# Kernel optimization log

Hardware: AMD Instinct MI355X
Metric: run time of the kernel (lower is better)

Reference implementation:

```python
import jax, jax.numpy as jnp
import numpy as np

B, T = 4096, 1024
IN, H, N, OUT = 1, 40, 40, 1  # input_size, hidden_size, nr_nodes, output_size
SLOPE = 0.01  # LeakyReLU negative slope (torch default)


def setup_inputs() -> dict:
    key = jax.random.key(0)
    ks = jax.random.split(key, 9)
    s = lambda fan_in: 1.0 / np.sqrt(fan_in)
    u = lambda k, shape, fan_in: jax.random.uniform(k, shape, jnp.float32, -s(fan_in), s(fan_in))
    return {
        "inputs": jax.random.normal(ks[0], (B, T), dtype=jnp.float32),
        # H2H: Linear(41->40), LeakyReLU, Linear(40->40)
        "h2h_w1": u(ks[1], (N, IN + H), IN + H),
        "h2h_b1": u(ks[2], (N,), IN + H),
        "h2h_w2": u(ks[3], (H, N), N),
        "h2h_b2": u(ks[4], (H,), N),
        # H2O: Linear(41->40), LeakyReLU, Linear(40->1)
        "h2o_w1": u(ks[5], (N, IN + H), IN + H),
        "h2o_b1": u(ks[6], (N,), IN + H),
        "h2o_w2": u(ks[7], (OUT, N), N),
        "h2o_b2": u(ks[8], (OUT,), N),
    }


def reference(inputs, h2h_w1, h2h_b1, h2h_w2, h2h_b2, h2o_w1, h2o_b1, h2o_w2, h2o_b2):
    def step(hidden, u_t):
        # combined: [B, 1+H]
        combined = jnp.concatenate([u_t[:, None], hidden], axis=1)
        a = jax.nn.leaky_relu(combined @ h2h_w1.T + h2h_b1, SLOPE)
        hidden_new = a @ h2h_w2.T + h2h_b2                      # [B, H]
        o = jax.nn.leaky_relu(combined @ h2o_w1.T + h2o_b1, SLOPE)
        out_t = (o @ h2o_w2.T + h2o_b2)[:, 0]                   # [B]
        return hidden_new, out_t

    hidden0 = jnp.zeros((inputs.shape[0], H), dtype=inputs.dtype)
    _, ys = jax.lax.scan(step, hidden0, inputs.T)  # ys: [T, B]
    return ys.T  # [B, T]
```

## Files before the change

### kernel.cpp

```cpp
#include <hip/hip_runtime.h>
#include <hip/hip_bf16.h>


#define B_SZ 4096
#define T_SZ 1024
#define HID  40

typedef unsigned short u16;
typedef unsigned int   u32;
typedef float f2 __attribute__((ext_vector_type(2)));

__device__ __forceinline__ float bf2f(u16 v) {
  union { u32 u; float f; } c; c.u = ((u32)v) << 16; return c.f;
}

template <bool BF>
__device__ __forceinline__ float ldg(const void* p, long i) {
  if (BF) return bf2f(((const u16*)p)[i]);
  return ((const float*)p)[i];
}

template <bool BF>
__device__ __forceinline__ f2 ldg2(const void* p, long i) {
  f2 r;
  r.x = ldg<BF>(p, i + 0);
  r.y = ldg<BF>(p, i + 1);
  return r;
}

__device__ __forceinline__ bool detect_bf16(const void* w) {
  const u16* p = (const u16*)w;
  bool bf = true;
  for (int i = 0; i < 64; ++i) {
    float f = bf2f(p[i]);
    if (!(fabsf(f) <= 0.2f)) bf = false;
  }
  return bf;
}

template <bool BF>
__global__ __launch_bounds__(128, 2)
void rnn_kernel(const void* __restrict__ inp,
                const void* __restrict__ h2h_w1, const void* __restrict__ h2h_b1,
                const void* __restrict__ h2h_w2, const void* __restrict__ h2h_b2,
                const void* __restrict__ h2o_w1, const void* __restrict__ h2o_b1,
                const void* __restrict__ h2o_w2, const void* __restrict__ h2o_b2,
                void* __restrict__ out) {
  __shared__ __align__(16) float sH[4][44];
  __shared__ __align__(16) float sA[4][84];

  if (detect_bf16(h2h_w1) != BF) return;

  const int tid  = threadIdx.x;
  const int lane = tid & 63;
  const int wv   = tid >> 6;
  const int el   = lane & 3;
  const int w    = wv * 16 + (lane >> 2);

  const int a0 = (wv == 0) ? 3 * w : 48 + 2 * (w - 16);
  const int nA = (wv == 0) ? 3 : 2;
  const int rB = (wv == 0) ? ((w < 8) ? 32 + w : ((w == 8) ? 40 : -1)) : 2 * (w - 16);

  f2    wS[4][20];
  float wu[3] = {0, 0, 0}, ba[3] = {0, 0, 0}, bb[2] = {0, 0};
#pragma unroll
  for (int q = 0; q < 3; ++q) {
    if (q < nA) {
      const int  j  = a0 + q;
      const bool hh = (j < HID);
      const void* wb1 = hh ? h2h_w1 : h2o_w1;
      const long  jr  = hh ? j : (j - HID);
      wu[q] = ldg<BF>(wb1, jr * 41);
      ba[q] = ldg<BF>(hh ? h2h_b1 : h2o_b1, jr);
#pragma unroll
      for (int i = 0; i < 20; ++i)
        wS[q][i] = ldg2<BF>(wb1, jr * 41 + 1 + 2 * i);
    }
  }
  if (wv == 0) {
    if (rB >= 0) {
      const bool isout = (rB == 40);
      const void* wb2 = isout ? h2o_w2 : h2h_w2;
      const long  rr  = isout ? 0 : rB;
      bb[0] = isout ? ldg<BF>(h2o_b2, 0) : ldg<BF>(h2h_b2, rB);
#pragma unroll
      for (int i = 0; i < 20; ++i)
        wS[3][i] = ldg2<BF>(wb2, rr * 40 + 2 * i);
    }
  } else {
#pragma unroll
    for (int q = 0; q < 2; ++q) {
      const long r = rB + q;
      bb[q] = ldg<BF>(h2h_b2, r);
#pragma unroll
      for (int i = 0; i < 20; ++i)
        wS[2 + q][i] = ldg2<BF>(h2h_w2, r * 40 + 2 * i);
    }
  }

  for (int i = tid; i < 4 * 44; i += 128) ((float*)sH)[i] = 0.f;
  __syncthreads();

  const int  b    = blockIdx.x * 4 + el;
  const long base = (long)b * T_SZ;
  float u_cur = ldg<BF>(inp, base);

  for (int t = 0; t < T_SZ; ++t) {
    const float u_nxt = (t + 1 < T_SZ) ? ldg<BF>(inp, base + t + 1) : 0.f;

    f2 hv[20];
    {
      const f2* hp = (const f2*)sH[el];
#pragma unroll
      for (int i = 0; i < 20; ++i) hv[i] = hp[i];
    }
#pragma unroll
    for (int q = 0; q < 3; ++q) {
      if (q < nA) {
        f2 acc = {0.f, 0.f};
#pragma unroll
        for (int i = 0; i < 20; ++i)
          acc = hv[i] * wS[q][i] + acc;
        const float a = fmaf(u_cur, wu[q], ba[q]) + acc.x + acc.y;
        sA[el][a0 + q] = fmaxf(a, 0.01f * a);
      }
    }
    __syncthreads();

    if (wv == 1) {
      f2 av[20];
      {
        const f2* ap = (const f2*)sA[el];
#pragma unroll
        for (int i = 0; i < 20; ++i) av[i] = ap[i];
      }
#pragma unroll
      for (int q = 0; q < 2; ++q) {
        f2 acc = {0.f, 0.f};
#pragma unroll
        for (int i = 0; i < 20; ++i)
          acc = av[i] * wS[2 + q][i] + acc;
        sH[el][rB + q] = bb[q] + acc.x + acc.y;
      }
    } else if (rB >= 0) {
      const f2* ap = (const f2*)(&sA[el][(rB == 40) ? 40 : 0]);
      f2 av[20];
#pragma unroll
      for (int i = 0; i < 20; ++i) av[i] = ap[i];
      f2 acc = {0.f, 0.f};
#pragma unroll
      for (int i = 0; i < 20; ++i)
        acc = av[i] * wS[3][i] + acc;
      const float a2 = bb[0] + acc.x + acc.y;
      if (rB < HID) {
        sH[el][rB] = a2;
      } else {
        if (BF) ((__hip_bfloat16*)out)[base + t] = __float2bfloat16(a2);
        else    ((float*)out)[base + t] = a2;
      }
    }
    __syncthreads();

    u_cur = u_nxt;
  }
}

extern "C" void kernel_launch(void* const* d_in, const int* in_sizes, int n_in,
                              void* d_out, int out_size, void* d_ws, size_t ws_size,
                              hipStream_t stream) {
  (void)in_sizes; (void)n_in; (void)out_size; (void)d_ws; (void)ws_size;
  rnn_kernel<false><<<dim3(B_SZ / 4), dim3(128), 0, stream>>>(
      d_in[0], d_in[1], d_in[2], d_in[3], d_in[4],
      d_in[5], d_in[6], d_in[7], d_in[8], d_out);
  rnn_kernel<true><<<dim3(B_SZ / 4), dim3(128), 0, stream>>>(
      d_in[0], d_in[1], d_in[2], d_in[3], d_in[4],
      d_in[5], d_in[6], d_in[7], d_in[8], d_out);
}
```

Measured before the change: 742.7 us.

## Redistribute RNN matvec work across 256 threads per block with fewer rows each

Doubles the block from 128 to 256 threads, still covering 4 batch elements, and reassigns work. Each thread now computes one or two first-layer rows instead of two or three, and one second-layer row instead of up to two. This shortens the serial dependency chain per timestep and cuts register use, using split accumulators and hidden-state values read directly from shared memory. In exchange there are twice as many wavefronts per block synchronising every step, and some threads in the upper waves sit idle during the second phase.

```diff
diff --git a/kernel.cpp b/kernel.cpp
--- a/kernel.cpp
+++ b/kernel.cpp
@@ -39,7 +39,7 @@
 }
 
 template <bool BF>
-__global__ __launch_bounds__(128, 2)
+__global__ __launch_bounds__(256, 4)
 void rnn_kernel(const void* __restrict__ inp,
                 const void* __restrict__ h2h_w1, const void* __restrict__ h2h_b1,
                 const void* __restrict__ h2h_w2, const void* __restrict__ h2h_b2,
@@ -51,112 +51,103 @@
 
   if (detect_bf16(h2h_w1) != BF) return;
 
-  const int tid  = threadIdx.x;
-  const int lane = tid & 63;
-  const int wv   = tid >> 6;
-  const int el   = lane & 3;
-  const int w    = wv * 16 + (lane >> 2);
+  const int tid = threadIdx.x;
+  const int el  = tid & 3;
+  const int w   = tid >> 2;
+  const int wv  = tid >> 6;
+  const bool two = (wv == 0);
 
-  const int a0 = (wv == 0) ? 3 * w : 48 + 2 * (w - 16);
-  const int nA = (wv == 0) ? 3 : 2;
-  const int rB = (wv == 0) ? ((w < 8) ? 32 + w : ((w == 8) ? 40 : -1)) : 2 * (w - 16);
-
-  f2    wS[4][20];
-  float wu[3] = {0, 0, 0}, ba[3] = {0, 0, 0}, bb[2] = {0, 0};
+  f2    wS0[20];
+  float wu0, ba0;
+  {
+    const bool hh = (w < HID);
+    const void* w1p = hh ? h2h_w1 : h2o_w1;
+    const long  jr  = hh ? w : (w - HID);
+    wu0 = ldg<BF>(w1p, jr * 41);
+    ba0 = ldg<BF>(hh ? h2h_b1 : h2o_b1, jr);
 #pragma unroll
-  for (int q = 0; q < 3; ++q) {
-    if (q < nA) {
-      const int  j  = a0 + q;
-      const bool hh = (j < HID);
-      const void* wb1 = hh ? h2h_w1 : h2o_w1;
-      const long  jr  = hh ? j : (j - HID);
-      wu[q] = ldg<BF>(wb1, jr * 41);
-      ba[q] = ldg<BF>(hh ? h2h_b1 : h2o_b1, jr);
-#pragma unroll
-      for (int i = 0; i < 20; ++i)
-        wS[q][i] = ldg2<BF>(wb1, jr * 41 + 1 + 2 * i);
-    }
-  }
-  if (wv == 0) {
-    if (rB >= 0) {
-      const bool isout = (rB == 40);
-      const void* wb2 = isout ? h2o_w2 : h2h_w2;
-      const long  rr  = isout ? 0 : rB;
-      bb[0] = isout ? ldg<BF>(h2o_b2, 0) : ldg<BF>(h2h_b2, rB);
-#pragma unroll
-      for (int i = 0; i < 20; ++i)
-        wS[3][i] = ldg2<BF>(wb2, rr * 40 + 2 * i);
-    }
-  } else {
-#pragma unroll
-    for (int q = 0; q < 2; ++q) {
-      const long r = rB + q;
-      bb[q] = ldg<BF>(h2h_b2, r);
-#pragma unroll
-      for (int i = 0; i < 20; ++i)
-        wS[2 + q][i] = ldg2<BF>(h2h_w2, r * 40 + 2 * i);
-    }
+    for (int i = 0; i < 20; ++i)
+      wS0[i] = ldg2<BF>(w1p, jr * 41 + 1 + 2 * i);
   }
 
-  for (int i = tid; i < 4 * 44; i += 128) ((float*)sH)[i] = 0.f;
+  f2    wS1[20];
+  float wuX = 0.f, baX = 0.f, bbX = 0.f;
+#pragma unroll
+  for (int i = 0; i < 20; ++i) wS1[i] = (f2)0.f;
+  if (two) {
+    const long jr = 24 + w;
+    wuX = ldg<BF>(h2o_w1, jr * 41);
+    baX = ldg<BF>(h2o_b1, jr);
+#pragma unroll
+    for (int i = 0; i < 20; ++i)
+      wS1[i] = ldg2<BF>(h2o_w1, jr * 41 + 1 + 2 * i);
+  } else if (w <= 56) {
+    const bool isout = (w == 56);
+    const void* w2p = isout ? h2o_w2 : h2h_w2;
+    const long  rr  = isout ? 0 : (w - 16);
+    bbX = isout ? ldg<BF>(h2o_b2, 0) : ldg<BF>(h2h_b2, w - 16);
+#pragma unroll
+    for (int i = 0; i < 20; ++i)
+      wS1[i] = ldg2<BF>(w2p, rr * 40 + 2 * i);
+  }
+
+  for (int i = tid; i < 4 * 44; i += 256) ((float*)sH)[i] = 0.f;
   __syncthreads();
 
   const int  b    = blockIdx.x * 4 + el;
   const long base = (long)b * T_SZ;
   float u_cur = ldg<BF>(inp, base);
 
+  const f2* hp = (const f2*)sH[el];
+
   for (int t = 0; t < T_SZ; ++t) {
     const float u_nxt = (t + 1 < T_SZ) ? ldg<BF>(inp, base + t + 1) : 0.f;
 
-    f2 hv[20];
+    f2 ac00 = {0.f, 0.f}, ac01 = {0.f, 0.f};
+    f2 ac10 = {0.f, 0.f}, ac11 = {0.f, 0.f};
+#pragma unroll
+    for (int m = 0; m < 5; ++m) {
+      const f2 h0 = hp[4 * m + 0], h1 = hp[4 * m + 1];
+      const f2 h2 = hp[4 * m + 2], h3 = hp[4 * m + 3];
+      ac00 = h0 * wS0[4 * m + 0] + ac00;
+      ac00 = h1 * wS0[4 * m + 1] + ac00;
+      ac01 = h2 * wS0[4 * m + 2] + ac01;
+      ac01 = h3 * wS0[4 * m + 3] + ac01;
+      if (two) {
+        ac10 = h0 * wS1[4 * m + 0] + ac10;
+        ac10 = h1 * wS1[4 * m + 1] + ac10;
+        ac11 = h2 * wS1[4 * m + 2] + ac11;
+        ac11 = h3 * wS1[4 * m + 3] + ac11;
+      }
+    }
     {
-      const f2* hp = (const f2*)sH[el];
-#pragma unroll
-      for (int i = 0; i < 20; ++i) hv[i] = hp[i];
+      const float a0 = fmaf(u_cur, wu0, ba0) + ac00.x + ac00.y + ac01.x + ac01.y;
+      sA[el][w] = fmaxf(a0, 0.01f * a0);
     }
-#pragma unroll
-    for (int q = 0; q < 3; ++q) {
-      if (q < nA) {
-        f2 acc = {0.f, 0.f};
-#pragma unroll
-        for (int i = 0; i < 20; ++i)
-          acc = hv[i] * wS[q][i] + acc;
-        const float a = fmaf(u_cur, wu[q], ba[q]) + acc.x + acc.y;
-        sA[el][a0 + q] = fmaxf(a, 0.01f * a);
-      }
+    if (two) {
+      const float a1 = fmaf(u_cur, wuX, baX) + ac10.x + ac10.y + ac11.x + ac11.y;
+      sA[el][64 + w] = fmaxf(a1, 0.01f * a1);
     }
     __syncthreads();
 
-    if (wv == 1) {
-      f2 av[20];
-      {
-        const f2* ap = (const f2*)sA[el];
+    if (!two && w <= 56) {
+      const f2* ap = (const f2*)(&sA[el][(w == 56) ? 40 : 0]);
+      f2 bc0 = {0.f, 0.f}, bc1 = {0.f, 0.f};
 #pragma unroll
-        for (int i = 0; i < 20; ++i) av[i] = ap[i];
+      for (int m = 0; m < 5; ++m) {
+        const f2 a0 = ap[4 * m + 0], a1 = ap[4 * m + 1];
+        const f2 a2 = ap[4 * m + 2], a3 = ap[4 * m + 3];
+        bc0 = a0 * wS1[4 * m + 0] + bc0;
+        bc0 = a1 * wS1[4 * m + 1] + bc0;
+        bc1 = a2 * wS1[4 * m + 2] + bc1;
+        bc1 = a3 * wS1[4 * m + 3] + bc1;
       }
-#pragma unroll
-      for (int q = 0; q < 2; ++q) {
-        f2 acc = {0.f, 0.f};
-#pragma unroll
-        for (int i = 0; i < 20; ++i)
-          acc = av[i] * wS[2 + q][i] + acc;
-        sH[el][rB + q] = bb[q] + acc.x + acc.y;
-      }
-    } else if (rB >= 0) {
-      const f2* ap = (const f2*)(&sA[el][(rB == 40) ? 40 : 0]);
-      f2 av[20];
-#pragma unroll
-      for (int i = 0; i < 20; ++i) av[i] = ap[i];
-      f2 acc = {0.f, 0.f};
-#pragma unroll
-      for (int i = 0; i < 20; ++i)
-        acc = av[i] * wS[3][i] + acc;
-      const float a2 = bb[0] + acc.x + acc.y;
-      if (rB < HID) {
-        sH[el][rB] = a2;
+      const float v = bbX + bc0.x + bc0.y + bc1.x + bc1.y;
+      if (w < 56) {
+        sH[el][w - 16] = v;
       } else {
-        if (BF) ((__hip_bfloat16*)out)[base + t] = __float2bfloat16(a2);
-        else    ((float*)out)[base + t] = a2;
+        if (BF) ((__hip_bfloat16*)out)[base + t] = __float2bfloat16(v);
+        else    ((float*)out)[base + t] = v;
       }
     }
     __syncthreads();
@@ -169,10 +160,10 @@
                               void* d_out, int out_size, void* d_ws, size_t ws_size,
                               hipStream_t stream) {
   (void)in_sizes; (void)n_in; (void)out_size; (void)d_ws; (void)ws_size;
-  rnn_kernel<false><<<dim3(B_SZ / 4), dim3(128), 0, stream>>>(
+  rnn_kernel<false><<<dim3(B_SZ / 4), dim3(256), 0, stream>>>(
       d_in[0], d_in[1], d_in[2], d_in[3], d_in[4],
       d_in[5], d_in[6], d_in[7], d_in[8], d_out);
-  rnn_kernel<true><<<dim3(B_SZ / 4), dim3(128), 0, stream>>>(
+  rnn_kernel<true><<<dim3(B_SZ / 4), dim3(256), 0, stream>>>(
       d_in[0], d_in[1], d_in[2], d_in[3], d_in[4],
       d_in[5], d_in[6], d_in[7], d_in[8], d_out);
 }
```

Result: slower. 1.903 ms (+156.3%).

## Map one batch row per block with split-K pairs and DPP reduction

Applied to the files above, without the earlier changes.

Each block now handles a single batch element instead of four. Each pair of threads splits the 40-wide dot products in half and combines the halves with a DPP lane swap. Part of the output branch's first layer (rows 24-39) moves into the second phase, with the final output projection deferred one step and double-buffered hidden and output state, to balance work across the two barriers. This shortens each thread's serial chain per timestep, at the cost of four times as many blocks, more redundant weight loads per block, and lower batch reuse of the register-held weights.

```diff
diff --git a/kernel.cpp b/kernel.cpp
--- a/kernel.cpp
+++ b/kernel.cpp
@@ -38,6 +38,11 @@
   return bf;
 }
 
+__device__ __forceinline__ float pair_other(float x) {
+  return __int_as_float(__builtin_amdgcn_update_dpp(
+      0, __float_as_int(x), 0xB1, 0xF, 0xF, true));
+}
+
 template <bool BF>
 __global__ __launch_bounds__(128, 2)
 void rnn_kernel(const void* __restrict__ inp,
@@ -46,122 +51,129 @@
                 const void* __restrict__ h2o_w1, const void* __restrict__ h2o_b1,
                 const void* __restrict__ h2o_w2, const void* __restrict__ h2o_b2,
                 void* __restrict__ out) {
-  __shared__ __align__(16) float sH[4][44];
-  __shared__ __align__(16) float sA[4][84];
+  __shared__ __align__(16) float sH[2][40];
+  __shared__ __align__(16) float sA[44];
+  __shared__ __align__(16) float sO[2][40];
 
   if (detect_bf16(h2h_w1) != BF) return;
 
   const int tid  = threadIdx.x;
-  const int lane = tid & 63;
-  const int wv   = tid >> 6;
-  const int el   = lane & 3;
-  const int w    = wv * 16 + (lane >> 2);
+  const int kh   = tid & 1;
+  const int p    = tid >> 1;
+  const int koff = kh * 20;
 
-  const int a0 = (wv == 0) ? 3 * w : 48 + 2 * (w - 16);
-  const int nA = (wv == 0) ? 3 : 2;
-  const int rB = (wv == 0) ? ((w < 8) ? 32 + w : ((w == 8) ? 40 : -1)) : 2 * (w - 16);
-
-  f2    wS[4][20];
-  float wu[3] = {0, 0, 0}, ba[3] = {0, 0, 0}, bb[2] = {0, 0};
+  f2    w1s[10];
+  float wu1, ba1;
+  {
+    const bool hh = (p < HID);
+    const void* wp = hh ? h2h_w1 : h2o_w1;
+    const long  jr = hh ? p : (p - HID);
+    wu1 = (kh == 0) ? ldg<BF>(wp, jr * 41) : 0.f;
+    ba1 = (kh == 0) ? ldg<BF>(hh ? h2h_b1 : h2o_b1, jr) : 0.f;
 #pragma unroll
-  for (int q = 0; q < 3; ++q) {
-    if (q < nA) {
-      const int  j  = a0 + q;
-      const bool hh = (j < HID);
-      const void* wb1 = hh ? h2h_w1 : h2o_w1;
-      const long  jr  = hh ? j : (j - HID);
-      wu[q] = ldg<BF>(wb1, jr * 41);
-      ba[q] = ldg<BF>(hh ? h2h_b1 : h2o_b1, jr);
-#pragma unroll
-      for (int i = 0; i < 20; ++i)
-        wS[q][i] = ldg2<BF>(wb1, jr * 41 + 1 + 2 * i);
-    }
-  }
-  if (wv == 0) {
-    if (rB >= 0) {
-      const bool isout = (rB == 40);
-      const void* wb2 = isout ? h2o_w2 : h2h_w2;
-      const long  rr  = isout ? 0 : rB;
-      bb[0] = isout ? ldg<BF>(h2o_b2, 0) : ldg<BF>(h2h_b2, rB);
-#pragma unroll
-      for (int i = 0; i < 20; ++i)
-        wS[3][i] = ldg2<BF>(wb2, rr * 40 + 2 * i);
-    }
-  } else {
-#pragma unroll
-    for (int q = 0; q < 2; ++q) {
-      const long r = rB + q;
-      bb[q] = ldg<BF>(h2h_b2, r);
-#pragma unroll
-      for (int i = 0; i < 20; ++i)
-        wS[2 + q][i] = ldg2<BF>(h2h_w2, r * 40 + 2 * i);
-    }
+    for (int i = 0; i < 10; ++i)
+      w1s[i] = ldg2<BF>(wp, jr * 41 + 1 + koff + 2 * i);
   }
 
-  for (int i = tid; i < 4 * 44; i += 128) ((float*)sH)[i] = 0.f;
+  f2    w2s[10];
+  float wu2 = 0.f, bb2 = 0.f;
+#pragma unroll
+  for (int i = 0; i < 10; ++i) w2s[i] = (f2)0.f;
+  if (p < HID) {
+    if (kh == 0) bb2 = ldg<BF>(h2h_b2, p);
+#pragma unroll
+    for (int i = 0; i < 10; ++i)
+      w2s[i] = ldg2<BF>(h2h_w2, (long)p * HID + koff + 2 * i);
+  } else if (p < 56) {
+    const long jr = 24 + (p - 40);
+    if (kh == 0) { wu2 = ldg<BF>(h2o_w1, jr * 41); bb2 = ldg<BF>(h2o_b1, jr); }
+#pragma unroll
+    for (int i = 0; i < 10; ++i)
+      w2s[i] = ldg2<BF>(h2o_w1, jr * 41 + 1 + koff + 2 * i);
+  } else if (p == 56) {
+    if (kh == 0) bb2 = ldg<BF>(h2o_b2, 0);
+#pragma unroll
+    for (int i = 0; i < 10; ++i)
+      w2s[i] = ldg2<BF>(h2o_w2, koff + 2 * i);
+  }
+
+  for (int i = tid; i < 80; i += 128) { ((float*)sH)[i] = 0.f; ((float*)sO)[i] = 0.f; }
+  if (tid < 44) sA[tid] = 0.f;
   __syncthreads();
 
-  const int  b    = blockIdx.x * 4 + el;
-  const long base = (long)b * T_SZ;
+  const long base = (long)blockIdx.x * T_SZ;
   float u_cur = ldg<BF>(inp, base);
 
+  const f2* h_rd0 = (const f2*)(&sH[0][koff]);
+  const f2* h_rd1 = (const f2*)(&sH[1][koff]);
+  float* w1p0 = (p < HID) ? &sA[p] : &sO[0][p - HID];
+  float* w1p1 = (p < HID) ? &sA[p] : &sO[1][p - HID];
+  const f2* r20 = (p < HID)  ? (const f2*)(&sA[koff])
+                : (p < 56)   ? (const f2*)(&sH[0][koff])
+                : (p == 56)  ? (const f2*)(&sO[1][koff])
+                             : (const f2*)(&sA[koff]);
+  const f2* r21 = (p < HID)  ? (const f2*)(&sA[koff])
+                : (p < 56)   ? (const f2*)(&sH[1][koff])
+                : (p == 56)  ? (const f2*)(&sO[0][koff])
+                             : (const f2*)(&sA[koff]);
+  float* w2p0 = (p < HID) ? &sH[1][p] : (p < 56 ? &sO[0][24 + (p - 40)] : &sA[40]);
+  float* w2p1 = (p < HID) ? &sH[0][p] : (p < 56 ? &sO[1][24 + (p - 40)] : &sA[40]);
+  const bool leaky2 = (p >= HID) && (p < 56);
+  const bool wr2    = (kh == 0) && (p < 56);
+  const bool wrY    = (kh == 0) && (p == 56);
+
   for (int t = 0; t < T_SZ; ++t) {
+    const bool odd = (t & 1);
     const float u_nxt = (t + 1 < T_SZ) ? ldg<BF>(inp, base + t + 1) : 0.f;
 
-    f2 hv[20];
     {
-      const f2* hp = (const f2*)sH[el];
+      const f2* hp = odd ? h_rd1 : h_rd0;
+      f2 hv[10];
 #pragma unroll
-      for (int i = 0; i < 20; ++i) hv[i] = hp[i];
-    }
+      for (int i = 0; i < 10; ++i) hv[i] = hp[i];
+      f2 acc = {0.f, 0.f};
 #pragma unroll
-    for (int q = 0; q < 3; ++q) {
-      if (q < nA) {
-        f2 acc = {0.f, 0.f};
-#pragma unroll
-        for (int i = 0; i < 20; ++i)
-          acc = hv[i] * wS[q][i] + acc;
-        const float a = fmaf(u_cur, wu[q], ba[q]) + acc.x + acc.y;
-        sA[el][a0 + q] = fmaxf(a, 0.01f * a);
-      }
+      for (int i = 0; i < 10; ++i) acc = hv[i] * w1s[i] + acc;
+      const float s1 = fmaf(u_cur, wu1, ba1) + acc.x + acc.y;
+      const float t1 = s1 + pair_other(s1);
+      const float a1 = fmaxf(t1, 0.01f * t1);
+      if (kh == 0) *(odd ? w1p1 : w1p0) = a1;
     }
     __syncthreads();
 
-    if (wv == 1) {
-      f2 av[20];
-      {
-        const f2* ap = (const f2*)sA[el];
+    {
+      const f2* rp = odd ? r21 : r20;
+      f2 av[10];
 #pragma unroll
-        for (int i = 0; i < 20; ++i) av[i] = ap[i];
-      }
-#pragma unroll
-      for (int q = 0; q < 2; ++q) {
-        f2 acc = {0.f, 0.f};
-#pragma unroll
-        for (int i = 0; i < 20; ++i)
-          acc = av[i] * wS[2 + q][i] + acc;
-        sH[el][rB + q] = bb[q] + acc.x + acc.y;
-      }
-    } else if (rB >= 0) {
-      const f2* ap = (const f2*)(&sA[el][(rB == 40) ? 40 : 0]);
-      f2 av[20];
-#pragma unroll
-      for (int i = 0; i < 20; ++i) av[i] = ap[i];
+      for (int i = 0; i < 10; ++i) av[i] = rp[i];
       f2 acc = {0.f, 0.f};
 #pragma unroll
-      for (int i = 0; i < 20; ++i)
-        acc = av[i] * wS[3][i] + acc;
-      const float a2 = bb[0] + acc.x + acc.y;
-      if (rB < HID) {
-        sH[el][rB] = a2;
-      } else {
-        if (BF) ((__hip_bfloat16*)out)[base + t] = __float2bfloat16(a2);
-        else    ((float*)out)[base + t] = a2;
+      for (int i = 0; i < 10; ++i) acc = av[i] * w2s[i] + acc;
+      const float s2 = fmaf(u_cur, wu2, bb2) + acc.x + acc.y;
+      const float t2 = s2 + pair_other(s2);
+      const float v2 = leaky2 ? fmaxf(t2, 0.01f * t2) : t2;
+      if (wr2) *(odd ? w2p1 : w2p0) = v2;
+      if (wrY && t > 0) {
+        if (BF) ((__hip_bfloat16*)out)[base + t - 1] = __float2bfloat16(v2);
+        else    ((float*)out)[base + t - 1] = v2;
       }
     }
     __syncthreads();
 
     u_cur = u_nxt;
+  }
+
+  if (p == 56) {
+    const f2* rp = (const f2*)(&sO[1][koff]);
+    f2 acc = {0.f, 0.f};
+#pragma unroll
+    for (int i = 0; i < 10; ++i) acc = rp[i] * w2s[i] + acc;
+    const float s2 = bb2 + acc.x + acc.y;
+    const float t2 = s2 + pair_other(s2);
+    if (kh == 0) {
+      if (BF) ((__hip_bfloat16*)out)[base + T_SZ - 1] = __float2bfloat16(t2);
+      else    ((float*)out)[base + T_SZ - 1] = t2;
+    }
   }
 }
 
@@ -169,10 +181,10 @@
                               void* d_out, int out_size, void* d_ws, size_t ws_size,
                               hipStream_t stream) {
   (void)in_sizes; (void)n_in; (void)out_size; (void)d_ws; (void)ws_size;
-  rnn_kernel<false><<<dim3(B_SZ / 4), dim3(128), 0, stream>>>(
+  rnn_kernel<false><<<dim3(B_SZ), dim3(128), 0, stream>>>(
       d_in[0], d_in[1], d_in[2], d_in[3], d_in[4],
       d_in[5], d_in[6], d_in[7], d_in[8], d_out);
-  rnn_kernel<true><<<dim3(B_SZ / 4), dim3(128), 0, stream>>>(
+  rnn_kernel<true><<<dim3(B_SZ), dim3(128), 0, stream>>>(
       d_in[0], d_in[1], d_in[2], d_in[3], d_in[4],
       d_in[5], d_in[6], d_in[7], d_in[8], d_out);
 }
```

Result: slower. 1.335 ms (+79.8%).
